# Kernel tuning notes

Hardware: AMD Instinct MI355X
Metric: run time of the kernel (lower is better)

The kernel has to match this reference:

```python
import jax, jax.numpy as jnp
import numpy as np

L = 6; H = 6; E = 384; HS = 64; T = 256; B = 64; V = 65; EPS = 1e-5


def _ln(x, g, b):
    m = x.mean(-1, keepdims=True)
    v = ((x - m) ** 2).mean(-1, keepdims=True)
    return (x - m) / jnp.sqrt(v + EPS) * g + b


def setup_inputs() -> dict:
    key = jax.random.key(0)
    ks = jax.random.split(key, 16)
    p = lambda k, s: jax.random.normal(k, s, jnp.float32) * 0.02
    inp = {
        'idx': jax.random.randint(ks[0], (B, T), 0, V),
        'targets': jax.random.randint(ks[1], (B, T), 0, V),
        'tok_emb': p(ks[2], (V, E)),
        'pos_emb': p(ks[3], (T, E)),
        'Wq': p(ks[4], (L, H, E, HS)),
        'Wk': p(ks[5], (L, H, E, HS)),
        'Wv': p(ks[6], (L, H, E, HS)),
        'Wproj': p(ks[7], (L, E, E)),
        'bproj': jnp.zeros((L, E), jnp.float32),
        'ln1_g': jnp.ones((L, E), jnp.float32),
        'ln1_b': jnp.zeros((L, E), jnp.float32),
        'ln2_g': jnp.ones((L, E), jnp.float32),
        'ln2_b': jnp.zeros((L, E), jnp.float32),
        'W1': p(ks[8], (L, E, 4 * E)),
        'b1': jnp.zeros((L, 4 * E), jnp.float32),
        'W2': p(ks[9], (L, 4 * E, E)),
        'b2': jnp.zeros((L, E), jnp.float32),
        'lnf_g': jnp.ones((E,), jnp.float32),
        'lnf_b': jnp.zeros((E,), jnp.float32),
        'Wlm': p(ks[10], (E, V)),
        'blm': jnp.zeros((V,), jnp.float32),
    }
    return inp


def reference(idx, targets, tok_emb, pos_emb, Wq, Wk, Wv, Wproj, bproj,
              ln1_g, ln1_b, ln2_g, ln2_b, W1, b1, W2, b2,
              lnf_g, lnf_b, Wlm, blm):
    Bx, Tx = idx.shape
    x = tok_emb[idx] + pos_emb[:Tx]            # [B,T,E]
    mask = jnp.tril(jnp.ones((Tx, Tx), bool))
    scale = E ** (-0.5)                        # NOTE: uses N_EMBED, not head_size (faithful to source)
    for l in range(L):
        h = _ln(x, ln1_g[l], ln1_b[l])
        q = jnp.einsum('bte,hes->bhts', h, Wq[l])
        k = jnp.einsum('bte,hes->bhts', h, Wk[l])
        v = jnp.einsum('bte,hes->bhts', h, Wv[l])
        w = jnp.einsum('bhts,bhus->bhtu', q, k) * scale
        w = jnp.where(mask, w, -jnp.inf)
        a = jax.nn.softmax(w, axis=-1)
        o = jnp.einsum('bhtu,bhus->bhts', a, v)
        o = o.transpose(0, 2, 1, 3).reshape(Bx, Tx, E)  # concat heads
        x = x + o @ Wproj[l] + bproj[l]
        h2 = _ln(x, ln2_g[l], ln2_b[l])
        x = x + jax.nn.relu(h2 @ W1[l] + b1[l]) @ W2[l] + b2[l]
    x = _ln(x, lnf_g, lnf_b)
    logits = x @ Wlm + blm                     # [B,T,V]
    logp = jax.nn.log_softmax(logits, axis=-1)
    loss = -jnp.take_along_axis(logp, targets[..., None], axis=-1).mean()
    return logits, loss
```

## Files before the change

kernel.cpp:

```cpp
#include <hip/hip_runtime.h>
#include <hip/hip_bf16.h>

typedef unsigned short u16;
typedef __attribute__((ext_vector_type(8))) unsigned short us8;
typedef __attribute__((ext_vector_type(8))) short mfma_in8;
typedef __attribute__((ext_vector_type(4))) float f32x4;

#define NL 6
#define NH 6
#define NE 384
#define NHS 64
#define NT 256
#define NB 64
#define NV 65
#define NM (NB * NT)
#define SCALE 0.051031036307982884f
#define LDP 40
#define VTP 264
#define PSP 44

static __device__ __forceinline__ float bf2f(u16 u) {
    return __uint_as_float(((unsigned int)u) << 16);
}
static __device__ __forceinline__ u16 f2bf(float f) {
    unsigned int x = __float_as_uint(f);
    unsigned int r = x + 0x7fffu + ((x >> 16) & 1u);
    return (u16)(r >> 16);
}
static __device__ __forceinline__ void llds16(const u16* g, u16* l) {
    __builtin_amdgcn_global_load_lds(
        (const __attribute__((address_space(1))) void*)g,
        (__attribute__((address_space(3))) void*)l, 16, 0, 0);
}

__global__ __launch_bounds__(256)
void embed_kernel(const int* __restrict__ idx, const float* __restrict__ tok,
                  const float* __restrict__ pos, float* __restrict__ x) {
    int gid = blockIdx.x * 256 + threadIdx.x;
    int bt = gid / NE, e = gid % NE;
    int t = bt & (NT - 1);
    x[gid] = tok[idx[bt] * NE + e] + pos[t * NE + e];
}

__global__ __launch_bounds__(256)
void ln_kernel(const float* __restrict__ x, const float* __restrict__ g,
               const float* __restrict__ b, u16* __restrict__ out) {
    const int wv = threadIdx.x >> 6, lane = threadIdx.x & 63;
    const int token = (blockIdx.x << 2) + wv;
    const float* row = x + (size_t)token * NE;
    float vals[6];
    float s = 0.f;
#pragma unroll
    for (int i = 0; i < 6; ++i) { vals[i] = row[i * 64 + lane]; s += vals[i]; }
#pragma unroll
    for (int off = 32; off >= 1; off >>= 1) s += __shfl_xor(s, off);
    float mean = s * (1.f / NE);
    float s2 = 0.f;
#pragma unroll
    for (int i = 0; i < 6; ++i) { float d = vals[i] - mean; s2 += d * d; }
#pragma unroll
    for (int off = 32; off >= 1; off >>= 1) s2 += __shfl_xor(s2, off);
    float inv = rsqrtf(s2 * (1.f / NE) + 1e-5f);
    u16* orow = out + (size_t)token * NE;
#pragma unroll
    for (int i = 0; i < 6; ++i) {
        int e = i * 64 + lane;
        orow[e] = f2bf((vals[i] - mean) * inv * g[e] + b[e]);
    }
}

__global__ __launch_bounds__(256)
void convQKV_kernel(const float* __restrict__ Wq, const float* __restrict__ Wk,
                    const float* __restrict__ Wv, u16* __restrict__ dst) {
    int i = blockIdx.x * 256 + threadIdx.x;
    int s = i & 63; int rest = i >> 6;
    int e = rest % NE; rest /= NE;
    int hh = rest % NH; rest /= NH;
    int which = rest % 3; int l = rest / 3;
    const float* W = which == 0 ? Wq : which == 1 ? Wk : Wv;
    float v = W[((size_t)(l * NH + hh) * NE + e) * NHS + s];
    dst[((size_t)l * 3 * NE + which * NE + hh * NHS + s) * NE + e] = f2bf(v);
}
__global__ __launch_bounds__(256)
void convT_kernel(const float* __restrict__ src, u16* __restrict__ dst,
                  int K, int N) {
    const float* s = src + (size_t)blockIdx.y * K * N;
    u16* d = dst + (size_t)blockIdx.y * K * N;
    int i = blockIdx.x * 256 + threadIdx.x;
    if (i >= K * N) return;
    int k = i / N, n = i % N;
    d[(size_t)n * K + k] = f2bf(s[i]);
}
__global__ __launch_bounds__(256)
void convLM_kernel(const float* __restrict__ Wlm, u16* __restrict__ dst) {
    int i = blockIdx.x * 256 + threadIdx.x;
    if (i >= 80 * NE) return;
    int n = i / NE, k = i % NE;
    dst[i] = f2bf(n < NV ? Wlm[(size_t)k * NV + n] : 0.f);
}

static __device__ __forceinline__ void gemm128_core(
        const u16* __restrict__ A, const u16* __restrict__ BT,
        int m0, int n0, int K, f32x4 acc[4][4]) {
    __shared__ __align__(16) u16 smA[128 * 32];
    __shared__ __align__(16) u16 smB[128 * 32];
    const int tid = threadIdx.x;
    const int wv = tid >> 6, lane = tid & 63;
    const int wm = wv & 1, wn = wv >> 1;
    const int quad = lane >> 4, l16 = lane & 15;
    for (int k0 = 0; k0 < K; k0 += 32) {
        __syncthreads();
#pragma unroll
        for (int j = 0; j < 2; ++j) {
            int c = tid + j * 256;
            llds16(A + (size_t)(m0 + (c >> 2)) * K + k0 + ((c & 3) << 3), smA + c * 8);
            llds16(BT + (size_t)(n0 + (c >> 2)) * K + k0 + ((c & 3) << 3), smB + c * 8);
        }
        __syncthreads();
        mfma_in8 af[4], bf[4];
#pragma unroll
        for (int im = 0; im < 4; ++im)
            af[im] = *(const mfma_in8*)&smA[(wm * 64 + im * 16 + l16) * 32 + quad * 8];
#pragma unroll
        for (int in = 0; in < 4; ++in)
            bf[in] = *(const mfma_in8*)&smB[(wn * 64 + in * 16 + l16) * 32 + quad * 8];
#pragma unroll
        for (int im = 0; im < 4; ++im)
#pragma unroll
            for (int in = 0; in < 4; ++in)
                acc[im][in] = __builtin_amdgcn_mfma_f32_16x16x32_bf16(
                    af[im], bf[in], acc[im][in], 0, 0, 0);
    }
}

__global__ __launch_bounds__(256)
void gemm_qkv_f(const u16* __restrict__ A, const u16* __restrict__ BT,
                u16* __restrict__ qout, u16* __restrict__ kout,
                u16* __restrict__ vout) {
    const int nbm = NM >> 7;
    const int bm = blockIdx.x % nbm, bn = blockIdx.x / nbm;
    const int m0 = bm << 7, n0 = bn << 7;
    f32x4 acc[4][4] = {};
    gemm128_core(A, BT, m0, n0, NE, acc);
    const int lane = threadIdx.x & 63, wv = threadIdx.x >> 6;
    const int wm = wv & 1, wn = wv >> 1;
    const int quad = lane >> 4, l16 = lane & 15;
#pragma unroll
    for (int im = 0; im < 4; ++im)
#pragma unroll
        for (int in = 0; in < 4; ++in)
#pragma unroll
            for (int r = 0; r < 4; ++r) {
                int row = m0 + wm * 64 + im * 16 + quad * 4 + r;
                int col = n0 + wn * 64 + in * 16 + l16;
                int which = col / NE, j = col % NE;
                int hh = j >> 6, s = j & 63;
                int bb = row >> 8, tt = row & 255;
                u16* dst = (which == 0) ? qout : (which == 1) ? kout : vout;
                dst[((((size_t)bb * NH + hh) << 8) + tt) * NHS + s] =
                    f2bf(acc[im][in][r]);
            }
}

__global__ __launch_bounds__(256)
void gemm_resid_f(const u16* __restrict__ A, const u16* __restrict__ BT,
                  const int N, const int K,
                  const float* __restrict__ bias, float* __restrict__ resid) {
    const int nbm = NM >> 7;
    const int bm = blockIdx.x % nbm, bn = blockIdx.x / nbm;
    const int m0 = bm << 7, n0 = bn << 7;
    f32x4 acc[4][4] = {};
    gemm128_core(A, BT, m0, n0, K, acc);
    const int lane = threadIdx.x & 63, wv = threadIdx.x >> 6;
    const int wm = wv & 1, wn = wv >> 1;
    const int quad = lane >> 4, l16 = lane & 15;
#pragma unroll
    for (int im = 0; im < 4; ++im)
#pragma unroll
        for (int in = 0; in < 4; ++in)
#pragma unroll
            for (int r = 0; r < 4; ++r) {
                int row = m0 + wm * 64 + im * 16 + quad * 4 + r;
                int col = n0 + wn * 64 + in * 16 + l16;
                resid[(size_t)row * N + col] += acc[im][in][r] + bias[col];
            }
}

__global__ __launch_bounds__(256)
void gemm_relu_f(const u16* __restrict__ A, const u16* __restrict__ BT,
                 const int N, const int K,
                 const float* __restrict__ bias, u16* __restrict__ outb) {
    const int nbm = NM >> 7;
    const int bm = blockIdx.x % nbm, bn = blockIdx.x / nbm;
    const int m0 = bm << 7, n0 = bn << 7;
    f32x4 acc[4][4] = {};
    gemm128_core(A, BT, m0, n0, K, acc);
    const int lane = threadIdx.x & 63, wv = threadIdx.x >> 6;
    const int wm = wv & 1, wn = wv >> 1;
    const int quad = lane >> 4, l16 = lane & 15;
#pragma unroll
    for (int im = 0; im < 4; ++im)
#pragma unroll
        for (int in = 0; in < 4; ++in)
#pragma unroll
            for (int r = 0; r < 4; ++r) {
                int row = m0 + wm * 64 + im * 16 + quad * 4 + r;
                int col = n0 + wn * 64 + in * 16 + l16;
                outb[(size_t)row * N + col] =
                    f2bf(fmaxf(acc[im][in][r] + bias[col], 0.f));
            }
}

__global__ __launch_bounds__(256)
void lmhead_f(const u16* __restrict__ xf, const u16* __restrict__ WlmT,
              const float* __restrict__ blm, float* __restrict__ out) {
    const int w = threadIdx.x >> 6, lane = threadIdx.x & 63;
    const int quad = lane >> 4, l16 = lane & 15;
    const int m0 = (blockIdx.x * 4 + w) * 16;
    f32x4 acc[5] = {};
#pragma unroll 2
    for (int k0 = 0; k0 < NE; k0 += 32) {
        mfma_in8 a = *(const mfma_in8*)(xf + (size_t)(m0 + l16) * NE + k0 + quad * 8);
#pragma unroll
        for (int nt = 0; nt < 5; ++nt) {
            mfma_in8 b = *(const mfma_in8*)(WlmT + (size_t)(nt * 16 + l16) * NE + k0 + quad * 8);
            acc[nt] = __builtin_amdgcn_mfma_f32_16x16x32_bf16(a, b, acc[nt], 0, 0, 0);
        }
    }
#pragma unroll
    for (int nt = 0; nt < 5; ++nt) {
        int col = nt * 16 + l16;
        if (col < NV) {
            float bb = blm[col];
#pragma unroll
            for (int r = 0; r < 4; ++r)
                out[(size_t)(m0 + quad * 4 + r) * NV + col] = acc[nt][r] + bb;
        }
    }
}

struct TileAcc { f32x4 acc[4][2]; };
static __device__ __forceinline__ void gemm_tile_core(
        const u16* __restrict__ A, const float* __restrict__ Bb,
        int m0, int nb0, int K, int ldb, TileAcc& T) {
    __shared__ __align__(16) u16 smA[128 * LDP];
    __shared__ __align__(16) u16 smB[64 * LDP];
    const int tid = threadIdx.x;
    const int wv = tid >> 6, lane = tid & 63;
    const int wm = wv & 1, wn = wv >> 1;
    const int quad = lane >> 4, l16 = lane & 15;
    const u16* Ab = A + (size_t)m0 * K;
    const int ar = tid >> 2, ac = (tid & 3) << 3;
    const int bk = tid >> 3, bc = (tid & 7) << 3;
    for (int k0 = 0; k0 < K; k0 += 32) {
        us8 a0 = *(const us8*)(Ab + (size_t)ar * K + k0 + ac);
        us8 a1 = *(const us8*)(Ab + (size_t)(ar + 64) * K + k0 + ac);
        const float* bp = Bb + (size_t)(k0 + bk) * ldb + nb0 + bc;
        float4 bv0 = *(const float4*)bp;
        float4 bv1 = *(const float4*)(bp + 4);
        __syncthreads();
        *(us8*)&smA[ar * LDP + ac] = a0;
        *(us8*)&smA[(ar + 64) * LDP + ac] = a1;
        smB[(bc + 0) * LDP + bk] = f2bf(bv0.x);
        smB[(bc + 1) * LDP + bk] = f2bf(bv0.y);
        smB[(bc + 2) * LDP + bk] = f2bf(bv0.z);
        smB[(bc + 3) * LDP + bk] = f2bf(bv0.w);
        smB[(bc + 4) * LDP + bk] = f2bf(bv1.x);
        smB[(bc + 5) * LDP + bk] = f2bf(bv1.y);
        smB[(bc + 6) * LDP + bk] = f2bf(bv1.z);
        smB[(bc + 7) * LDP + bk] = f2bf(bv1.w);
        __syncthreads();
        mfma_in8 af[4], bfr[2];
#pragma unroll
        for (int im = 0; im < 4; ++im)
            af[im] = *(const mfma_in8*)&smA[(wm * 64 + im * 16 + l16) * LDP + quad * 8];
#pragma unroll
        for (int in = 0; in < 2; ++in)
            bfr[in] = *(const mfma_in8*)&smB[(wn * 32 + in * 16 + l16) * LDP + quad * 8];
#pragma unroll
        for (int im = 0; im < 4; ++im)
#pragma unroll
            for (int in = 0; in < 2; ++in)
                T.acc[im][in] = __builtin_amdgcn_mfma_f32_16x16x32_bf16(
                    af[im], bfr[in], T.acc[im][in], 0, 0, 0);
    }
}
__global__ __launch_bounds__(256)
void gemm_qkv_kernel(const u16* __restrict__ A,
                     const float* __restrict__ B0, const float* __restrict__ B1,
                     const float* __restrict__ B2,
                     u16* __restrict__ qout, u16* __restrict__ kout,
                     u16* __restrict__ vout) {
    const int nbm = NM >> 7;
    const int bm = blockIdx.x % nbm, bn = blockIdx.x / nbm;
    const int m0 = bm << 7;
    const int which = bn / NH, hh = bn % NH;
    const float* Bb = (which == 0 ? B0 : which == 1 ? B1 : B2) + (size_t)hh * NE * NHS;
    TileAcc T = {};
    gemm_tile_core(A, Bb, m0, 0, NE, NHS, T);
    const int lane = threadIdx.x & 63, wv = threadIdx.x >> 6;
    const int wm = wv & 1, wn = wv >> 1;
    const int quad = lane >> 4, l16 = lane & 15;
    u16* dst = (which == 0) ? qout : (which == 1) ? kout : vout;
#pragma unroll
    for (int im = 0; im < 4; ++im)
#pragma unroll
        for (int in = 0; in < 2; ++in)
#pragma unroll
            for (int r = 0; r < 4; ++r) {
                int row = m0 + wm * 64 + im * 16 + quad * 4 + r;
                int s = wn * 32 + in * 16 + l16;
                int bb = row >> 8, tt = row & 255;
                dst[((((size_t)bb * NH + hh) << 8) + tt) * NHS + s] =
                    f2bf(T.acc[im][in][r]);
            }
}
__global__ __launch_bounds__(256)
void gemm_resid_kernel(const u16* __restrict__ A, const float* __restrict__ B,
                       const int N, const int K,
                       const float* __restrict__ bias, float* __restrict__ resid) {
    const int nbm = NM >> 7;
    const int bm = blockIdx.x % nbm, bn = blockIdx.x / nbm;
    const int m0 = bm << 7, n0 = bn << 6;
    TileAcc T = {};
    gemm_tile_core(A, B, m0, n0, K, N, T);
    const int lane = threadIdx.x & 63, wv = threadIdx.x >> 6;
    const int wm = wv & 1, wn = wv >> 1;
    const int quad = lane >> 4, l16 = lane & 15;
#pragma unroll
    for (int im = 0; im < 4; ++im)
#pragma unroll
        for (int in = 0; in < 2; ++in)
#pragma unroll
            for (int r = 0; r < 4; ++r) {
                int row = m0 + wm * 64 + im * 16 + quad * 4 + r;
                int col = n0 + wn * 32 + in * 16 + l16;
                resid[(size_t)row * N + col] += T.acc[im][in][r] + bias[col];
            }
}
__global__ __launch_bounds__(256)
void gemm_relu_kernel(const u16* __restrict__ A, const float* __restrict__ B,
                      const int N, const int K,
                      const float* __restrict__ bias, u16* __restrict__ outb) {
    const int nbm = NM >> 7;
    const int bm = blockIdx.x % nbm, bn = blockIdx.x / nbm;
    const int m0 = bm << 7, n0 = bn << 6;
    TileAcc T = {};
    gemm_tile_core(A, B, m0, n0, K, N, T);
    const int lane = threadIdx.x & 63, wv = threadIdx.x >> 6;
    const int wm = wv & 1, wn = wv >> 1;
    const int quad = lane >> 4, l16 = lane & 15;
#pragma unroll
    for (int im = 0; im < 4; ++im)
#pragma unroll
        for (int in = 0; in < 2; ++in)
#pragma unroll
            for (int r = 0; r < 4; ++r) {
                int row = m0 + wm * 64 + im * 16 + quad * 4 + r;
                int col = n0 + wn * 32 + in * 16 + l16;
                outb[(size_t)row * N + col] =
                    f2bf(fmaxf(T.acc[im][in][r] + bias[col], 0.f));
            }
}
__global__ __launch_bounds__(256)
void lmhead_kernel(const u16* __restrict__ xf, const float* __restrict__ Wlm,
                   const float* __restrict__ blm, float* __restrict__ out) {
    int gid = blockIdx.x * 256 + threadIdx.x;
    int m = gid / NV, vv = gid % NV;
    const u16* xr = xf + (size_t)m * NE;
    float acc = blm[vv];
#pragma unroll 4
    for (int kk = 0; kk < NE; ++kk)
        acc += bf2f(xr[kk]) * Wlm[kk * NV + vv];
    out[gid] = acc;
}

static __device__ __forceinline__ f32x4 shflx4(f32x4 v, int off) {
    f32x4 r;
#pragma unroll
    for (int i = 0; i < 4; ++i) r[i] = __shfl_xor(v[i], off);
    return r;
}
__global__ __launch_bounds__(256)
void attn_kernel(const u16* __restrict__ q, const u16* __restrict__ k,
                 const u16* __restrict__ v, u16* __restrict__ o) {
    __shared__ __align__(16) u16 sVt[64 * VTP];
    __shared__ __align__(16) u16 sP[4][16 * PSP];
    const int tid = threadIdx.x;
    const int bh = blockIdx.x;
    const int b = bh / NH, hh = bh % NH;
    const size_t base = (size_t)bh << 14;
    {
        const us8* vg = (const us8*)(v + base);
        const int t0 = tid >> 3, c8 = tid & 7;
#pragma unroll
        for (int i = 0; i < 8; ++i) {
            int tt = t0 + i * 32;
            us8 vv = vg[tt * 8 + c8];
#pragma unroll
            for (int j = 0; j < 8; ++j)
                sVt[(c8 * 8 + j) * VTP + tt] = vv[j];
        }
    }
    __syncthreads();
    const int w = tid >> 6, lane = tid & 63;
    const int quad = lane >> 4, l16 = lane & 15;
    mfma_in8 aq[4][2];
#pragma unroll
    for (int mt = 0; mt < 4; ++mt) {
        const int t = w + 4 * mt;
        const u16* qp = q + base + (size_t)(16 * t + l16) * NHS + quad * 8;
        aq[mt][0] = *(const mfma_in8*)qp;
        aq[mt][1] = *(const mfma_in8*)(qp + 32);
    }
    f32x4 oa[4][4] = {};
    f32x4 lsum[4] = {};
    const f32x4 zero = {};
    const int jmax = ((w + 12) >> 1) + 1;
    for (int j = 0; j < jmax; ++j) {
        mfma_in8 bv[4];
#pragma unroll
        for (int nt = 0; nt < 4; ++nt)
            bv[nt] = *(const mfma_in8*)&sVt[(nt * 16 + l16) * VTP + j * 32 + quad * 8];
        mfma_in8 bk[2][2];
#pragma unroll
        for (int nt = 0; nt < 2; ++nt) {
            const u16* kp = k + base + (size_t)(j * 32 + nt * 16 + l16) * NHS + quad * 8;
            bk[nt][0] = *(const mfma_in8*)kp;
            bk[nt][1] = *(const mfma_in8*)(kp + 32);
        }
#pragma unroll
        for (int mt = 0; mt < 4; ++mt) {
            const int t = w + 4 * mt;
            const int jm = t >> 1;
            if (j > jm) continue;
            f32x4 s0 = __builtin_amdgcn_mfma_f32_16x16x32_bf16(aq[mt][0], bk[0][0], zero, 0, 0, 0);
            s0 = __builtin_amdgcn_mfma_f32_16x16x32_bf16(aq[mt][1], bk[0][1], s0, 0, 0, 0);
            f32x4 s1 = __builtin_amdgcn_mfma_f32_16x16x32_bf16(aq[mt][0], bk[1][0], zero, 0, 0, 0);
            s1 = __builtin_amdgcn_mfma_f32_16x16x32_bf16(aq[mt][1], bk[1][1], s1, 0, 0, 0);
            float p[2][4];
            const bool boundary = (j == jm);
#pragma unroll
            for (int nt = 0; nt < 2; ++nt)
#pragma unroll
                for (int r = 0; r < 4; ++r) {
                    float sv = (nt ? s1[r] : s0[r]) * SCALE;
                    float e = __expf(sv);
                    if (boundary) {
                        int u = j * 32 + nt * 16 + l16;
                        int R = 16 * t + quad * 4 + r;
                        if (u > R) e = 0.f;
                    }
                    p[nt][r] = e;
                }
            f32x4 rs;
#pragma unroll
            for (int r = 0; r < 4; ++r) rs[r] = p[0][r] + p[1][r];
            rs += shflx4(rs, 1);
            rs += shflx4(rs, 2);
            rs += shflx4(rs, 4);
            rs += shflx4(rs, 8);
            lsum[mt] += rs;
#pragma unroll
            for (int nt = 0; nt < 2; ++nt)
#pragma unroll
                for (int r = 0; r < 4; ++r)
                    sP[w][(quad * 4 + r) * PSP + nt * 16 + l16] = f2bf(p[nt][r]);
            mfma_in8 ap = *(const mfma_in8*)&sP[w][l16 * PSP + quad * 8];
#pragma unroll
            for (int nt = 0; nt < 4; ++nt)
                oa[mt][nt] = __builtin_amdgcn_mfma_f32_16x16x32_bf16(ap, bv[nt], oa[mt][nt], 0, 0, 0);
        }
    }
#pragma unroll
    for (int mt = 0; mt < 4; ++mt) {
        const int t = w + 4 * mt;
        f32x4 inv;
#pragma unroll
        for (int r = 0; r < 4; ++r) inv[r] = 1.f / lsum[mt][r];
#pragma unroll
        for (int nt = 0; nt < 4; ++nt)
#pragma unroll
            for (int r = 0; r < 4; ++r) {
                int row = 16 * t + quad * 4 + r;
                int col = hh * NHS + nt * 16 + l16;
                o[((size_t)(b * NT + row)) * NE + col] = f2bf(oa[mt][nt][r] * inv[r]);
            }
    }
}

__global__ __launch_bounds__(256)
void loss_kernel(const float* __restrict__ logits, const int* __restrict__ targets,
                 float* __restrict__ acc) {
    int t = blockIdx.x * 256 + threadIdx.x;
    const float* row = logits + (size_t)t * NV;
    float mx = -1e30f;
    for (int i = 0; i < NV; ++i) mx = fmaxf(mx, row[i]);
    float se = 0.f;
    for (int i = 0; i < NV; ++i) se += __expf(row[i] - mx);
    float li = __logf(se) + mx - row[targets[t]];
#pragma unroll
    for (int off = 32; off >= 1; off >>= 1) li += __shfl_xor(li, off);
    if ((threadIdx.x & 63) == 0) atomicAdd(acc, li);
}
__global__ void loss_final_kernel(const float* __restrict__ acc, float* __restrict__ out) {
    out[0] = acc[0] * (1.f / (float)NM);
}
__global__ void code_kernel(float* __restrict__ out0, float code) {
    if (threadIdx.x == 0 && blockIdx.x == 0) out0[0] = code;
}

extern "C" void kernel_launch(void* const* d_in, const int* in_sizes, int n_in,
                              void* d_out, int out_size, void* d_ws, size_t ws_size,
                              hipStream_t stream) {
    const int*   idx      = (const int*)d_in[0];
    const int*   targets  = (const int*)d_in[1];
    const float* tok_emb  = (const float*)d_in[2];
    const float* pos_emb  = (const float*)d_in[3];
    const float* Wq       = (const float*)d_in[4];
    const float* Wk       = (const float*)d_in[5];
    const float* Wv       = (const float*)d_in[6];
    const float* Wproj    = (const float*)d_in[7];
    const float* bproj    = (const float*)d_in[8];
    const float* ln1_g    = (const float*)d_in[9];
    const float* ln1_b    = (const float*)d_in[10];
    const float* ln2_g    = (const float*)d_in[11];
    const float* ln2_b    = (const float*)d_in[12];
    const float* W1       = (const float*)d_in[13];
    const float* b1       = (const float*)d_in[14];
    const float* W2       = (const float*)d_in[15];
    const float* b2       = (const float*)d_in[16];
    const float* lnf_g    = (const float*)d_in[17];
    const float* lnf_b    = (const float*)d_in[18];
    const float* Wlm      = (const float*)d_in[19];
    const float* blm      = (const float*)d_in[20];
    float* out = (float*)d_out;

    static const int expect[21] = {
        16384, 16384, 24960, 98304, 884736, 884736, 884736, 884736, 2304,
        2304, 2304, 2304, 2304, 3538944, 9216, 3538944, 2304, 384, 384,
        24960, 65};
    if (n_in < 21) { code_kernel<<<1, 1, 0, stream>>>(out, 990.f); return; }
    for (int i = 0; i < 21; ++i)
        if (in_sizes[i] != expect[i]) {
            code_kernel<<<1, 1, 0, stream>>>(out, 1000.f + 10.f * i);
            return;
        }

    char* ws = (char*)d_ws;
    size_t off = 0;
    auto alloc = [&](size_t bytes) -> void* {
        void* p = ws + off;
        off += (bytes + 255) & ~(size_t)255;
        return p;
    };
    const size_t S = (size_t)NM * NE * 2;
    float* lossacc = (float*)alloc(256);
    float* x       = (float*)alloc((size_t)NM * NE * 4);
    u16*   h       = (u16*)alloc(S);
    u16*   region  = (u16*)alloc(4 * S);
    u16*   qb = region;
    u16*   kb = region + NM * NE;
    u16*   vb = region + 2 * (size_t)NM * NE;
    u16*   ob = region + 3 * (size_t)NM * NE;
    u16*   ub = region;
    const size_t base_need = off;
    u16* WqkvT  = (u16*)alloc((size_t)NL * 3 * NE * NE * 2);
    u16* WprojT = (u16*)alloc((size_t)NL * NE * NE * 2);
    u16* W1T    = (u16*)alloc((size_t)NL * NE * 4 * NE * 2);
    u16* W2T    = (u16*)alloc((size_t)NL * NE * 4 * NE * 2);
    u16* WlmT   = (u16*)alloc((size_t)80 * NE * 2);
    const size_t fast_need = off;

    const bool fast = (ws_size >= fast_need);
    if (!fast && ws_size < base_need) {
        code_kernel<<<1, 1, 0, stream>>>(out, 999.f);
        return;
    }

    hipMemsetAsync(lossacc, 0, 4, stream);
    embed_kernel<<<(NM * NE) / 256, 256, 0, stream>>>(idx, tok_emb, pos_emb, x);

    if (fast) {
        convQKV_kernel<<<(NL * 3 * NH * NE * NHS) / 256, 256, 0, stream>>>(Wq, Wk, Wv, WqkvT);
        convT_kernel<<<dim3((NE * NE + 255) / 256, NL), 256, 0, stream>>>(Wproj, WprojT, NE, NE);
        convT_kernel<<<dim3((NE * 4 * NE + 255) / 256, NL), 256, 0, stream>>>(W1, W1T, NE, 4 * NE);
        convT_kernel<<<dim3((NE * 4 * NE + 255) / 256, NL), 256, 0, stream>>>(W2, W2T, 4 * NE, NE);
        convLM_kernel<<<(80 * NE + 255) / 256, 256, 0, stream>>>(Wlm, WlmT);
    }

    const int gLN = NM / 4;
    const int nbm = NM / 128;
    for (int l = 0; l < NL; ++l) {
        ln_kernel<<<gLN, 256, 0, stream>>>(x, ln1_g + l * NE, ln1_b + l * NE, h);
        if (fast) {
            gemm_qkv_f<<<nbm * (3 * NE / 128), 256, 0, stream>>>(
                h, WqkvT + (size_t)l * 3 * NE * NE, qb, kb, vb);
        } else {
            const size_t wqkv = (size_t)l * NH * NE * NHS;
            gemm_qkv_kernel<<<nbm * (3 * NE / 64), 256, 0, stream>>>(
                h, Wq + wqkv, Wk + wqkv, Wv + wqkv, qb, kb, vb);
        }
        attn_kernel<<<NB * NH, 256, 0, stream>>>(qb, kb, vb, ob);
        if (fast) {
            gemm_resid_f<<<nbm * (NE / 128), 256, 0, stream>>>(
                ob, WprojT + (size_t)l * NE * NE, NE, NE, bproj + l * NE, x);
        } else {
            gemm_resid_kernel<<<nbm * (NE / 64), 256, 0, stream>>>(
                ob, Wproj + (size_t)l * NE * NE, NE, NE, bproj + l * NE, x);
        }
        ln_kernel<<<gLN, 256, 0, stream>>>(x, ln2_g + l * NE, ln2_b + l * NE, h);
        if (fast) {
            gemm_relu_f<<<nbm * (4 * NE / 128), 256, 0, stream>>>(
                h, W1T + (size_t)l * NE * 4 * NE, 4 * NE, NE, b1 + l * 4 * NE, ub);
            gemm_resid_f<<<nbm * (NE / 128), 256, 0, stream>>>(
                ub, W2T + (size_t)l * NE * 4 * NE, NE, 4 * NE, b2 + l * NE, x);
        } else {
            gemm_relu_kernel<<<nbm * (4 * NE / 64), 256, 0, stream>>>(
                h, W1 + (size_t)l * NE * 4 * NE, 4 * NE, NE, b1 + l * 4 * NE, ub);
            gemm_resid_kernel<<<nbm * (NE / 64), 256, 0, stream>>>(
                ub, W2 + (size_t)l * NE * 4 * NE, NE, 4 * NE, b2 + l * NE, x);
        }
    }

    ln_kernel<<<gLN, 256, 0, stream>>>(x, lnf_g, lnf_b, h);
    if (fast)
        lmhead_f<<<NM / 64, 256, 0, stream>>>(h, WlmT, blm, out);
    else
        lmhead_kernel<<<(NM * NV) / 256, 256, 0, stream>>>(h, Wlm, blm, out);
    loss_kernel<<<NM / 256, 256, 0, stream>>>(out, targets, lossacc);
    if (out_size > NM * NV)
        loss_final_kernel<<<1, 1, 0, stream>>>(lossacc, out + (size_t)NM * NV);
}
```

Baseline: 1.324 ms.

## Store residual stream in bf16, vectorize layernorm, use 128x64 tiles for residual GEMMs

The residual stream x is now kept in bf16 instead of fp32, which halves its memory traffic in embed, layernorm and the residual-add GEMM epilogues. Layernorm is rewritten so that 16 threads handle one token and each moves 24 elements through 16-byte vector loads and stores. The residual GEMMs switch to a 128x64 tile core with direct global-to-LDS loads, giving more blocks for N=384. The unused slow fallback kernels are removed. Accumulating the residual in bf16 across 6 layers adds rounding error, which may matter against the fp32 reference tolerance.

New measurement: 1.213 ms. -8.4%, faster.

```diff
diff --git a/kernel.cpp b/kernel.cpp
--- a/kernel.cpp
+++ b/kernel.cpp
@@ -15,7 +15,6 @@
 #define NV 65
 #define NM (NB * NT)
 #define SCALE 0.051031036307982884f
-#define LDP 40
 #define VTP 264
 #define PSP 44
 
@@ -35,38 +34,52 @@
 
 __global__ __launch_bounds__(256)
 void embed_kernel(const int* __restrict__ idx, const float* __restrict__ tok,
-                  const float* __restrict__ pos, float* __restrict__ x) {
+                  const float* __restrict__ pos, u16* __restrict__ x) {
     int gid = blockIdx.x * 256 + threadIdx.x;
     int bt = gid / NE, e = gid % NE;
     int t = bt & (NT - 1);
-    x[gid] = tok[idx[bt] * NE + e] + pos[t * NE + e];
-}
-
-__global__ __launch_bounds__(256)
-void ln_kernel(const float* __restrict__ x, const float* __restrict__ g,
+    x[gid] = f2bf(tok[idx[bt] * NE + e] + pos[t * NE + e]);
+}
+
+__global__ __launch_bounds__(256)
+void ln_kernel(const u16* __restrict__ x, const float* __restrict__ g,
                const float* __restrict__ b, u16* __restrict__ out) {
-    const int wv = threadIdx.x >> 6, lane = threadIdx.x & 63;
-    const int token = (blockIdx.x << 2) + wv;
-    const float* row = x + (size_t)token * NE;
-    float vals[6];
+    const int sub = threadIdx.x & 15;
+    const int token = blockIdx.x * 16 + (threadIdx.x >> 4);
+    const u16* row = x + (size_t)token * NE + sub * 24;
+    us8 v0 = *(const us8*)row;
+    us8 v1 = *(const us8*)(row + 8);
+    us8 v2 = *(const us8*)(row + 16);
+    float vals[24];
+#pragma unroll
+    for (int j = 0; j < 8; ++j) {
+        vals[j] = bf2f(v0[j]); vals[8 + j] = bf2f(v1[j]); vals[16 + j] = bf2f(v2[j]);
+    }
     float s = 0.f;
 #pragma unroll
-    for (int i = 0; i < 6; ++i) { vals[i] = row[i * 64 + lane]; s += vals[i]; }
-#pragma unroll
-    for (int off = 32; off >= 1; off >>= 1) s += __shfl_xor(s, off);
+    for (int j = 0; j < 24; ++j) s += vals[j];
+#pragma unroll
+    for (int off = 8; off >= 1; off >>= 1) s += __shfl_xor(s, off);
     float mean = s * (1.f / NE);
     float s2 = 0.f;
 #pragma unroll
-    for (int i = 0; i < 6; ++i) { float d = vals[i] - mean; s2 += d * d; }
-#pragma unroll
-    for (int off = 32; off >= 1; off >>= 1) s2 += __shfl_xor(s2, off);
+    for (int j = 0; j < 24; ++j) { float d = vals[j] - mean; s2 += d * d; }
+#pragma unroll
+    for (int off = 8; off >= 1; off >>= 1) s2 += __shfl_xor(s2, off);
     float inv = rsqrtf(s2 * (1.f / NE) + 1e-5f);
-    u16* orow = out + (size_t)token * NE;
-#pragma unroll
-    for (int i = 0; i < 6; ++i) {
-        int e = i * 64 + lane;
-        orow[e] = f2bf((vals[i] - mean) * inv * g[e] + b[e]);
-    }
+    const float* gp = g + sub * 24;
+    const float* bp = b + sub * 24;
+    us8 o0, o1, o2;
+#pragma unroll
+    for (int j = 0; j < 8; ++j) {
+        o0[j] = f2bf((vals[j] - mean) * inv * gp[j] + bp[j]);
+        o1[j] = f2bf((vals[8 + j] - mean) * inv * gp[8 + j] + bp[8 + j]);
+        o2[j] = f2bf((vals[16 + j] - mean) * inv * gp[16 + j] + bp[16 + j]);
+    }
+    u16* orow = out + (size_t)token * NE + sub * 24;
+    *(us8*)orow = o0;
+    *(us8*)(orow + 8) = o1;
+    *(us8*)(orow + 16) = o2;
 }
 
 __global__ __launch_bounds__(256)
@@ -163,30 +176,6 @@
 }
 
 __global__ __launch_bounds__(256)
-void gemm_resid_f(const u16* __restrict__ A, const u16* __restrict__ BT,
-                  const int N, const int K,
-                  const float* __restrict__ bias, float* __restrict__ resid) {
-    const int nbm = NM >> 7;
-    const int bm = blockIdx.x % nbm, bn = blockIdx.x / nbm;
-    const int m0 = bm << 7, n0 = bn << 7;
-    f32x4 acc[4][4] = {};
-    gemm128_core(A, BT, m0, n0, K, acc);
-    const int lane = threadIdx.x & 63, wv = threadIdx.x >> 6;
-    const int wm = wv & 1, wn = wv >> 1;
-    const int quad = lane >> 4, l16 = lane & 15;
-#pragma unroll
-    for (int im = 0; im < 4; ++im)
-#pragma unroll
-        for (int in = 0; in < 4; ++in)
-#pragma unroll
-            for (int r = 0; r < 4; ++r) {
-                int row = m0 + wm * 64 + im * 16 + quad * 4 + r;
-                int col = n0 + wn * 64 + in * 16 + l16;
-                resid[(size_t)row * N + col] += acc[im][in][r] + bias[col];
-            }
-}
-
-__global__ __launch_bounds__(256)
 void gemm_relu_f(const u16* __restrict__ A, const u16* __restrict__ BT,
                  const int N, const int K,
                  const float* __restrict__ bias, u16* __restrict__ outb) {
@@ -211,6 +200,63 @@
             }
 }
 
+static __device__ __forceinline__ void gemm64_core(
+        const u16* __restrict__ A, const u16* __restrict__ BT,
+        int m0, int n0, int K, f32x4 acc[4][2]) {
+    __shared__ __align__(16) u16 smA[128 * 32];
+    __shared__ __align__(16) u16 smB[64 * 32];
+    const int tid = threadIdx.x;
+    const int wv = tid >> 6, lane = tid & 63;
+    const int wm = wv & 1, wn = wv >> 1;
+    const int quad = lane >> 4, l16 = lane & 15;
+    for (int k0 = 0; k0 < K; k0 += 32) {
+        __syncthreads();
+        llds16(A + (size_t)(m0 + (tid >> 2)) * K + k0 + ((tid & 3) << 3), smA + tid * 8);
+        llds16(A + (size_t)(m0 + 64 + (tid >> 2)) * K + k0 + ((tid & 3) << 3),
+               smA + (tid + 256) * 8);
+        llds16(BT + (size_t)(n0 + (tid >> 2)) * K + k0 + ((tid & 3) << 3), smB + tid * 8);
+        __syncthreads();
+        mfma_in8 af[4], bf[2];
+#pragma unroll
+        for (int im = 0; im < 4; ++im)
+            af[im] = *(const mfma_in8*)&smA[(wm * 64 + im * 16 + l16) * 32 + quad * 8];
+#pragma unroll
+        for (int in = 0; in < 2; ++in)
+            bf[in] = *(const mfma_in8*)&smB[(wn * 32 + in * 16 + l16) * 32 + quad * 8];
+#pragma unroll
+        for (int im = 0; im < 4; ++im)
+#pragma unroll
+            for (int in = 0; in < 2; ++in)
+                acc[im][in] = __builtin_amdgcn_mfma_f32_16x16x32_bf16(
+                    af[im], bf[in], acc[im][in], 0, 0, 0);
+    }
+}
+
+__global__ __launch_bounds__(256)
+void gemm_resid_f(const u16* __restrict__ A, const u16* __restrict__ BT,
+                  const int N, const int K,
+                  const float* __restrict__ bias, u16* __restrict__ resid) {
+    const int nbm = NM >> 7;
+    const int bm = blockIdx.x % nbm, bn = blockIdx.x / nbm;
+    const int m0 = bm << 7, n0 = bn << 6;
+    f32x4 acc[4][2] = {};
+    gemm64_core(A, BT, m0, n0, K, acc);
+    const int lane = threadIdx.x & 63, wv = threadIdx.x >> 6;
+    const int wm = wv & 1, wn = wv >> 1;
+    const int quad = lane >> 4, l16 = lane & 15;
+#pragma unroll
+    for (int im = 0; im < 4; ++im)
+#pragma unroll
+        for (int in = 0; in < 2; ++in)
+#pragma unroll
+            for (int r = 0; r < 4; ++r) {
+                int row = m0 + wm * 64 + im * 16 + quad * 4 + r;
+                int col = n0 + wn * 32 + in * 16 + l16;
+                size_t o = (size_t)row * N + col;
+                resid[o] = f2bf(bf2f(resid[o]) + acc[im][in][r] + bias[col]);
+            }
+}
+
 __global__ __launch_bounds__(256)
 void lmhead_f(const u16* __restrict__ xf, const u16* __restrict__ WlmT,
               const float* __restrict__ blm, float* __restrict__ out) {
@@ -237,142 +283,6 @@
                 out[(size_t)(m0 + quad * 4 + r) * NV + col] = acc[nt][r] + bb;
         }
     }
-}
-
-struct TileAcc { f32x4 acc[4][2]; };
-static __device__ __forceinline__ void gemm_tile_core(
-        const u16* __restrict__ A, const float* __restrict__ Bb,
-        int m0, int nb0, int K, int ldb, TileAcc& T) {
-    __shared__ __align__(16) u16 smA[128 * LDP];
-    __shared__ __align__(16) u16 smB[64 * LDP];
-    const int tid = threadIdx.x;
-    const int wv = tid >> 6, lane = tid & 63;
-    const int wm = wv & 1, wn = wv >> 1;
-    const int quad = lane >> 4, l16 = lane & 15;
-    const u16* Ab = A + (size_t)m0 * K;
-    const int ar = tid >> 2, ac = (tid & 3) << 3;
-    const int bk = tid >> 3, bc = (tid & 7) << 3;
-    for (int k0 = 0; k0 < K; k0 += 32) {
-        us8 a0 = *(const us8*)(Ab + (size_t)ar * K + k0 + ac);
-        us8 a1 = *(const us8*)(Ab + (size_t)(ar + 64) * K + k0 + ac);
-        const float* bp = Bb + (size_t)(k0 + bk) * ldb + nb0 + bc;
-        float4 bv0 = *(const float4*)bp;
-        float4 bv1 = *(const float4*)(bp + 4);
-        __syncthreads();
-        *(us8*)&smA[ar * LDP + ac] = a0;
-        *(us8*)&smA[(ar + 64) * LDP + ac] = a1;
-        smB[(bc + 0) * LDP + bk] = f2bf(bv0.x);
-        smB[(bc + 1) * LDP + bk] = f2bf(bv0.y);
-        smB[(bc + 2) * LDP + bk] = f2bf(bv0.z);
-        smB[(bc + 3) * LDP + bk] = f2bf(bv0.w);
-        smB[(bc + 4) * LDP + bk] = f2bf(bv1.x);
-        smB[(bc + 5) * LDP + bk] = f2bf(bv1.y);
-        smB[(bc + 6) * LDP + bk] = f2bf(bv1.z);
-        smB[(bc + 7) * LDP + bk] = f2bf(bv1.w);
-        __syncthreads();
-        mfma_in8 af[4], bfr[2];
-#pragma unroll
-        for (int im = 0; im < 4; ++im)
-            af[im] = *(const mfma_in8*)&smA[(wm * 64 + im * 16 + l16) * LDP + quad * 8];
-#pragma unroll
-        for (int in = 0; in < 2; ++in)
-            bfr[in] = *(const mfma_in8*)&smB[(wn * 32 + in * 16 + l16) * LDP + quad * 8];
-#pragma unroll
-        for (int im = 0; im < 4; ++im)
-#pragma unroll
-            for (int in = 0; in < 2; ++in)
-                T.acc[im][in] = __builtin_amdgcn_mfma_f32_16x16x32_bf16(
-                    af[im], bfr[in], T.acc[im][in], 0, 0, 0);
-    }
-}
-__global__ __launch_bounds__(256)
-void gemm_qkv_kernel(const u16* __restrict__ A,
-                     const float* __restrict__ B0, const float* __restrict__ B1,
-                     const float* __restrict__ B2,
-                     u16* __restrict__ qout, u16* __restrict__ kout,
-                     u16* __restrict__ vout) {
-    const int nbm = NM >> 7;
-    const int bm = blockIdx.x % nbm, bn = blockIdx.x / nbm;
-    const int m0 = bm << 7;
-    const int which = bn / NH, hh = bn % NH;
-    const float* Bb = (which == 0 ? B0 : which == 1 ? B1 : B2) + (size_t)hh * NE * NHS;
-    TileAcc T = {};
-    gemm_tile_core(A, Bb, m0, 0, NE, NHS, T);
-    const int lane = threadIdx.x & 63, wv = threadIdx.x >> 6;
-    const int wm = wv & 1, wn = wv >> 1;
-    const int quad = lane >> 4, l16 = lane & 15;
-    u16* dst = (which == 0) ? qout : (which == 1) ? kout : vout;
-#pragma unroll
-    for (int im = 0; im < 4; ++im)
-#pragma unroll
-        for (int in = 0; in < 2; ++in)
-#pragma unroll
-            for (int r = 0; r < 4; ++r) {
-                int row = m0 + wm * 64 + im * 16 + quad * 4 + r;
-                int s = wn * 32 + in * 16 + l16;
-                int bb = row >> 8, tt = row & 255;
-                dst[((((size_t)bb * NH + hh) << 8) + tt) * NHS + s] =
-                    f2bf(T.acc[im][in][r]);
-            }
-}
-__global__ __launch_bounds__(256)
-void gemm_resid_kernel(const u16* __restrict__ A, const float* __restrict__ B,
-                       const int N, const int K,
-                       const float* __restrict__ bias, float* __restrict__ resid) {
-    const int nbm = NM >> 7;
-    const int bm = blockIdx.x % nbm, bn = blockIdx.x / nbm;
-    const int m0 = bm << 7, n0 = bn << 6;
-    TileAcc T = {};
-    gemm_tile_core(A, B, m0, n0, K, N, T);
-    const int lane = threadIdx.x & 63, wv = threadIdx.x >> 6;
-    const int wm = wv & 1, wn = wv >> 1;
-    const int quad = lane >> 4, l16 = lane & 15;
-#pragma unroll
-    for (int im = 0; im < 4; ++im)
-#pragma unroll
-        for (int in = 0; in < 2; ++in)
-#pragma unroll
-            for (int r = 0; r < 4; ++r) {
-                int row = m0 + wm * 64 + im * 16 + quad * 4 + r;
-                int col = n0 + wn * 32 + in * 16 + l16;
-                resid[(size_t)row * N + col] += T.acc[im][in][r] + bias[col];
-            }
-}
-__global__ __launch_bounds__(256)
-void gemm_relu_kernel(const u16* __restrict__ A, const float* __restrict__ B,
-                      const int N, const int K,
-                      const float* __restrict__ bias, u16* __restrict__ outb) {
-    const int nbm = NM >> 7;
-    const int bm = blockIdx.x % nbm, bn = blockIdx.x / nbm;
-    const int m0 = bm << 7, n0 = bn << 6;
-    TileAcc T = {};
-    gemm_tile_core(A, B, m0, n0, K, N, T);
-    const int lane = threadIdx.x & 63, wv = threadIdx.x >> 6;
-    const int wm = wv & 1, wn = wv >> 1;
-    const int quad = lane >> 4, l16 = lane & 15;
-#pragma unroll
-    for (int im = 0; im < 4; ++im)
-#pragma unroll
-        for (int in = 0; in < 2; ++in)
-#pragma unroll
-            for (int r = 0; r < 4; ++r) {
-                int row = m0 + wm * 64 + im * 16 + quad * 4 + r;
-                int col = n0 + wn * 32 + in * 16 + l16;
-                outb[(size_t)row * N + col] =
-                    f2bf(fmaxf(T.acc[im][in][r] + bias[col], 0.f));
-            }
-}
-__global__ __launch_bounds__(256)
-void lmhead_kernel(const u16* __restrict__ xf, const float* __restrict__ Wlm,
-                   const float* __restrict__ blm, float* __restrict__ out) {
-    int gid = blockIdx.x * 256 + threadIdx.x;
-    int m = gid / NV, vv = gid % NV;
-    const u16* xr = xf + (size_t)m * NE;
-    float acc = blm[vv];
-#pragma unroll 4
-    for (int kk = 0; kk < NE; ++kk)
-        acc += bf2f(xr[kk]) * Wlm[kk * NV + vv];
-    out[gid] = acc;
 }
 
 static __device__ __forceinline__ f32x4 shflx4(f32x4 v, int off) {
@@ -556,7 +466,7 @@
     };
     const size_t S = (size_t)NM * NE * 2;
     float* lossacc = (float*)alloc(256);
-    float* x       = (float*)alloc((size_t)NM * NE * 4);
+    u16*   x       = (u16*)alloc(S);
     u16*   h       = (u16*)alloc(S);
     u16*   region  = (u16*)alloc(4 * S);
     u16*   qb = region;
@@ -564,70 +474,41 @@
     u16*   vb = region + 2 * (size_t)NM * NE;
     u16*   ob = region + 3 * (size_t)NM * NE;
     u16*   ub = region;
-    const size_t base_need = off;
     u16* WqkvT  = (u16*)alloc((size_t)NL * 3 * NE * NE * 2);
     u16* WprojT = (u16*)alloc((size_t)NL * NE * NE * 2);
     u16* W1T    = (u16*)alloc((size_t)NL * NE * 4 * NE * 2);
     u16* W2T    = (u16*)alloc((size_t)NL * NE * 4 * NE * 2);
     u16* WlmT   = (u16*)alloc((size_t)80 * NE * 2);
-    const size_t fast_need = off;
-
-    const bool fast = (ws_size >= fast_need);
-    if (!fast && ws_size < base_need) {
-        code_kernel<<<1, 1, 0, stream>>>(out, 999.f);
-        return;
-    }
+
+    if (ws_size < off) { code_kernel<<<1, 1, 0, stream>>>(out, 999.f); return; }
 
     hipMemsetAsync(lossacc, 0, 4, stream);
     embed_kernel<<<(NM * NE) / 256, 256, 0, stream>>>(idx, tok_emb, pos_emb, x);
 
-    if (fast) {
-        convQKV_kernel<<<(NL * 3 * NH * NE * NHS) / 256, 256, 0, stream>>>(Wq, Wk, Wv, WqkvT);
-        convT_kernel<<<dim3((NE * NE + 255) / 256, NL), 256, 0, stream>>>(Wproj, WprojT, NE, NE);
-        convT_kernel<<<dim3((NE * 4 * NE + 255) / 256, NL), 256, 0, stream>>>(W1, W1T, NE, 4 * NE);
-        convT_kernel<<<dim3((NE * 4 * NE + 255) / 256, NL), 256, 0, stream>>>(W2, W2T, 4 * NE, NE);
-        convLM_kernel<<<(80 * NE + 255) / 256, 256, 0, stream>>>(Wlm, WlmT);
-    }
-
-    const int gLN = NM / 4;
+    convQKV_kernel<<<(NL * 3 * NH * NE * NHS) / 256, 256, 0, stream>>>(Wq, Wk, Wv, WqkvT);
+    convT_kernel<<<dim3((NE * NE + 255) / 256, NL), 256, 0, stream>>>(Wproj, WprojT, NE, NE);
+    convT_kernel<<<dim3((NE * 4 * NE + 255) / 256, NL), 256, 0, stream>>>(W1, W1T, NE, 4 * NE);
+    convT_kernel<<<dim3((NE * 4 * NE + 255) / 256, NL), 256, 0, stream>>>(W2, W2T, 4 * NE, NE);
+    convLM_kernel<<<(80 * NE + 255) / 256, 256, 0, stream>>>(Wlm, WlmT);
+
+    const int gLN = NM / 16;
     const int nbm = NM / 128;
     for (int l = 0; l < NL; ++l) {
         ln_kernel<<<gLN, 256, 0, stream>>>(x, ln1_g + l * NE, ln1_b + l * NE, h);
-        if (fast) {
-            gemm_qkv_f<<<nbm * (3 * NE / 128), 256, 0, stream>>>(
-                h, WqkvT + (size_t)l * 3 * NE * NE, qb, kb, vb);
-        } else {
-            const size_t wqkv = (size_t)l * NH * NE * NHS;
-            gemm_qkv_kernel<<<nbm * (3 * NE / 64), 256, 0, stream>>>(
-                h, Wq + wqkv, Wk + wqkv, Wv + wqkv, qb, kb, vb);
-        }
+        gemm_qkv_f<<<nbm * (3 * NE / 128), 256, 0, stream>>>(
+            h, WqkvT + (size_t)l * 3 * NE * NE, qb, kb, vb);
         attn_kernel<<<NB * NH, 256, 0, stream>>>(qb, kb, vb, ob);
-        if (fast) {
-            gemm_resid_f<<<nbm * (NE / 128), 256, 0, stream>>>(
-                ob, WprojT + (size_t)l * NE * NE, NE, NE, bproj + l * NE, x);
-        } else {
-            gemm_resid_kernel<<<nbm * (NE / 64), 256, 0, stream>>>(
-                ob, Wproj + (size_t)l * NE * NE, NE, NE, bproj + l * NE, x);
-        }
+        gemm_resid_f<<<nbm * (NE / 64), 256, 0, stream>>>(
+            ob, WprojT + (size_t)l * NE * NE, NE, NE, bproj + l * NE, x);
         ln_kernel<<<gLN, 256, 0, stream>>>(x, ln2_g + l * NE, ln2_b + l * NE, h);
-        if (fast) {
-            gemm_relu_f<<<nbm * (4 * NE / 128), 256, 0, stream>>>(
-                h, W1T + (size_t)l * NE * 4 * NE, 4 * NE, NE, b1 + l * 4 * NE, ub);
-            gemm_resid_f<<<nbm * (NE / 128), 256, 0, stream>>>(
-                ub, W2T + (size_t)l * NE * 4 * NE, NE, 4 * NE, b2 + l * NE, x);
-        } else {
-            gemm_relu_kernel<<<nbm * (4 * NE / 64), 256, 0, stream>>>(
-                h, W1 + (size_t)l * NE * 4 * NE, 4 * NE, NE, b1 + l * 4 * NE, ub);
-            gemm_resid_kernel<<<nbm * (NE / 64), 256, 0, stream>>>(
-                ub, W2 + (size_t)l * NE * 4 * NE, NE, 4 * NE, b2 + l * NE, x);
-        }
+        gemm_relu_f<<<nbm * (4 * NE / 128), 256, 0, stream>>>(
+            h, W1T + (size_t)l * NE * 4 * NE, 4 * NE, NE, b1 + l * 4 * NE, ub);
+        gemm_resid_f<<<nbm * (NE / 64), 256, 0, stream>>>(
+            ub, W2T + (size_t)l * NE * 4 * NE, NE, 4 * NE, b2 + l * NE, x);
     }
 
     ln_kernel<<<gLN, 256, 0, stream>>>(x, lnf_g, lnf_b, h);
-    if (fast)
-        lmhead_f<<<NM / 64, 256, 0, stream>>>(h, WlmT, blm, out);
-    else
-        lmhead_kernel<<<(NM * NV) / 256, 256, 0, stream>>>(h, Wlm, blm, out);
+    lmhead_f<<<NM / 64, 256, 0, stream>>>(h, WlmT, blm, out);
     loss_kernel<<<NM / 256, 256, 0, stream>>>(out, targets, lossacc);
     if (out_size > NM * NV)
         loss_final_kernel<<<1, 1, 0, stream>>>(lossacc, out + (size_t)NM * NV);
```
